# Kernel tuning notes

Measured on AMD Instinct MI355X. Metric: run time of the kernel, lower is better.

Reference implementation:

```python
import jax, jax.numpy as jnp
import numpy as np

N_TRAIN = 2000
N_ATOMS = 21
DIM_D = N_ATOMS * (N_ATOMS - 1) // 2   # 210 pairwise descriptors
DIM_I = 3 * N_ATOMS                    # 63 Cartesian force dims
N_PERMS = 12
N_COLS = 8
SIG = 10.0

_TRIL_ROWS, _TRIL_COLS = np.tril_indices(N_ATOMS, k=-1)


def setup_inputs() -> dict:
    key = jax.random.key(0)
    k1, k2 = jax.random.split(key)
    R_desc = jax.random.normal(k1, (N_TRAIN, DIM_D), dtype=jnp.float32)
    R_d_desc = jax.random.normal(k2, (N_TRAIN, DIM_D, 3), dtype=jnp.float32)
    rng = np.random.default_rng(0)
    # permutation table: identity first, then random symmetry perms of descriptor rows
    perms = np.stack([np.arange(DIM_D)] + [rng.permutation(DIM_D) for _ in range(N_PERMS - 1)])  # (P, D)
    # linear indices into a tiled (P copies) descriptor, laid out so that
    # tril_perms_lin.reshape(DIM_D, N_PERMS)[k, p] = perms[p, k] + p*DIM_D (matches sGDML)
    tril_perms_lin = (perms.T + np.arange(N_PERMS)[None, :] * DIM_D).ravel()
    j_idxs = rng.integers(0, N_TRAIN, size=N_COLS)
    return {
        "R_desc": R_desc,
        "R_d_desc": R_d_desc,
        "tril_perms_lin": jnp.asarray(tril_perms_lin, dtype=jnp.int32),
        "j_idxs": jnp.asarray(j_idxs, dtype=jnp.int32),
    }


def _d_desc_full(d_comp):
    """Expand compact pairwise Jacobian (N, D, 3) to full (N, D, 3*A).
    Pair row k for atoms (a,b) gets +d in atom a's slot and -d in atom b's slot."""
    n = d_comp.shape[0]
    out = jnp.zeros((n, DIM_D, N_ATOMS, 3), d_comp.dtype)
    k = jnp.arange(DIM_D)
    out = out.at[:, k, _TRIL_ROWS].set(d_comp)
    out = out.at[:, k, _TRIL_COLS].set(-d_comp)
    return out.reshape(n, DIM_D, DIM_I)


def reference(R_desc, R_d_desc, tril_perms_lin, j_idxs):
    sqrt5 = np.sqrt(5.0).astype(np.float32)
    base_div = 3.0 * SIG ** 4
    # indexing a P-fold tiled array of length D is equivalent to mod D
    perm_idx = jnp.reshape(tril_perms_lin, (DIM_D, N_PERMS)).T % DIM_D  # (P, D)
    Rd_full = _d_desc_full(R_d_desc)  # (N, D, I)

    def column_block(j):
        rj_desc_perms = R_desc[j][perm_idx]        # (P, D)  permuted descriptor of point j
        rj_d_perms = Rd_full[j][perm_idx]          # (P, D, I) permuted Jacobian of point j
        diff = R_desc[:, None, :] - rj_desc_perms[None, :, :]   # (N, P, D)
        norm = sqrt5 * jnp.linalg.norm(diff, axis=-1)            # (N, P)
        mat52 = jnp.exp(-norm / SIG) * (5.0 / base_div)          # (N, P)
        b = jnp.einsum('npd,pde->npe', diff, rj_d_perms)         # (N, P, I)
        outer = jnp.einsum('npd,npe->nde', diff * (5.0 * mat52)[..., None], b)  # (N, D, I)
        outer = outer - jnp.einsum('pde,np->nde', rj_d_perms, (SIG ** 2 + SIG * norm) * mat52)
        kblk = jnp.einsum('nde,ndk->nke', outer, Rd_full)        # (N, I_row, I_col)
        return kblk.reshape(N_TRAIN * DIM_I, DIM_I)

    K = jax.vmap(column_block)(j_idxs)                 # (nJ, N*I, I)
    K = jnp.transpose(K, (1, 0, 2)).reshape(N_TRAIN * DIM_I, N_COLS * DIM_I)
    return K
```

## Files before the change

kernel.cpp:

```cpp
#include <hip/hip_runtime.h>
#include <hip/hip_fp16.h>
#include <math.h>

#define NTRAIN 2000
#define DIMD 210
#define DIMI 63
#define NPERM 12
#define NCOLS 8
#define NATOM 21
#define SIGF 10.0f

#define WS_PERM      0
#define WS_PAIRROW   5040
#define WS_PAIRCOL   5250
#define WS_GTAB      6300
#define WS_ENTOFF    11340
#define WS_ENTS      11782
#define WS_TILEMAP   21862
#define WS_PERMAB    22304
#define A_INT_OFF    25088
#define A_BYTE_OFF   (A_INT_OFF * 4)
#define A_PER_N      (64 * 224)
#define A_BYTES      ((size_t)NTRAIN * A_PER_N * 2)
#define WS_NEEDED    ((size_t)A_BYTE_OFF + A_BYTES)

typedef _Float16 f16x8 __attribute__((ext_vector_type(8)));
typedef float f32x4 __attribute__((ext_vector_type(4)));

__global__ __launch_bounds__(512) void gdml_setup(const int* __restrict__ tril,
                                                  int* __restrict__ ws, int wsBig) {
  __shared__ int sPerm[NPERM * DIMD];
  __shared__ int sInv[NPERM * DIMD];
  __shared__ int sRow[DIMD], sCol[DIMD];
  __shared__ int sPairs[NATOM * 20], sNeg[NATOM * 20];
  __shared__ int sCnt[441];
  __shared__ int sScan[512];
  __shared__ int sOff[442];

  const int tid = threadIdx.x;

  for (int d = tid; d < DIMD; d += 512) {
    int a = 1;
    while ((a * (a + 1)) / 2 <= d) a++;
    sRow[d] = a;
    sCol[d] = d - (a * (a - 1)) / 2;
  }
  for (int idx = tid; idx < NPERM * DIMD; idx += 512) {
    int p = idx / DIMD, d = idx % DIMD;
    sPerm[idx] = tril[d * NPERM + p] % DIMD;
  }
  __syncthreads();
  for (int idx = tid; idx < NPERM * DIMD; idx += 512) {
    int p = idx / DIMD;
    sInv[p * DIMD + sPerm[idx]] = idx % DIMD;
  }
  if (tid < NATOM) {
    int t = tid, c = 0;
    for (int d = 0; d < DIMD; ++d) {
      if (sRow[d] == t)      { sPairs[t * 20 + c] = d; sNeg[t * 20 + c] = 0; c++; }
      else if (sCol[d] == t) { sPairs[t * 20 + c] = d; sNeg[t * 20 + c] = 1; c++; }
    }
  }
  __syncthreads();

  for (int idx = tid; idx < NPERM * DIMD; idx += 512) ws[WS_PERM + idx] = sPerm[idx];
  for (int d = tid; d < DIMD; d += 512) {
    ws[WS_PAIRROW + d] = sRow[d];
    ws[WS_PAIRCOL + d] = sCol[d];
  }
  for (int idx = tid; idx < NPERM * NATOM * 20; idx += 512) {
    int p = idx / (NATOM * 20);
    int r = idx % (NATOM * 20);
    int d = sPairs[r], neg = sNeg[r];
    int tw = sInv[p * DIMD + d];
    int pd = sPerm[p * DIMD + d];
    ws[WS_GTAB + idx] = d | (tw << 9) | (pd << 18) | (neg << 27);
  }
  if (wsBig) {
    for (int idx = tid; idx < NPERM * DIMD; idx += 512) {
      int dd = sPerm[idx];
      ws[WS_PERMAB + idx] = dd | (sRow[dd] << 8) | (sCol[dd] << 13);
    }
  }

  for (int q = tid; q < 441; q += 512) {
    int A = q / NATOM, B = q % NATOM, c = 0;
    for (int i = 0; i < 20; ++i) {
      int d = sPairs[A * 20 + i];
      for (int p = 0; p < NPERM; ++p) {
        int dd = sPerm[p * DIMD + d];
        c += (sRow[dd] == B) + (sCol[dd] == B);
      }
    }
    sCnt[q] = c;
  }
  __syncthreads();

  sScan[tid] = (tid < 441) ? sCnt[tid] : 0;
  __syncthreads();
  for (int s = 1; s < 512; s <<= 1) {
    int v = (tid >= s) ? sScan[tid - s] : 0;
    __syncthreads();
    sScan[tid] += v;
    __syncthreads();
  }
  if (tid == 0) sOff[0] = 0;
  if (tid < 441) sOff[tid + 1] = sScan[tid];
  __syncthreads();
  for (int q = tid; q < 442; q += 512) ws[WS_ENTOFF + q] = sOff[q];

  for (int q = tid; q < 441; q += 512) {
    int c = sCnt[q], r = 0;
    for (int q2 = 0; q2 < 441; ++q2) {
      int c2v = sCnt[q2];
      r += (c2v > c) || (c2v == c && q2 < q);
    }
    ws[WS_TILEMAP + r] = q;
  }

  for (int q = tid; q < 441; q += 512) {
    int A = q / NATOM, B = q % NATOM;
    int o = sOff[q];
    for (int i = 0; i < 20; ++i) {
      int d = sPairs[A * 20 + i];
      int negA = sNeg[A * 20 + i];
      for (int p = 0; p < NPERM; ++p) {
        int dd = sPerm[p * DIMD + d];
        int base = (d << 3) | (dd << 15) | (p << 26);
        if (sRow[dd] == B) ws[WS_ENTS + (o++)] = base | ((negA ^ 1) << 30);
        if (sCol[dd] == B) ws[WS_ENTS + (o++)] = base | (negA << 30);
      }
    }
  }
}

__global__ __launch_bounds__(256) void build_A(const float* __restrict__ R_d_desc,
                                               int* __restrict__ ws) {
  const int bid = blockIdx.x;
  const int n = (bid & 7) * (NTRAIN / 8) + (bid >> 3);
  const int* gtab = ws + WS_GTAB;
  _Float16* A = (_Float16*)((char*)ws + A_BYTE_OFF) + (size_t)n * A_PER_N;
  const float* rd = R_d_desc + (size_t)n * (DIMD * 3);
  const int tid = threadIdx.x;

  f16x8 z = {0, 0, 0, 0, 0, 0, 0, 0};
  for (int u = tid; u < 64 * 28; u += 256) ((f16x8*)A)[u] = z;
  __syncthreads();

  for (int u = tid; u < NATOM * 20; u += 256) {
    int v = gtab[u];
    int d = v & 511;
    float s = (v & (1 << 27)) ? -1.0f : 1.0f;
    int at = u / 20;
    A[(3 * at + 0) * 224 + d] = (_Float16)(s * rd[3 * d + 0]);
    A[(3 * at + 1) * 224 + d] = (_Float16)(s * rd[3 * d + 1]);
    A[(3 * at + 2) * 224 + d] = (_Float16)(s * rd[3 * d + 2]);
  }
}

__device__ inline unsigned h16(float f) {
  return (unsigned)__half_as_ushort(__float2half_rn(f));
}
__device__ inline float uh(unsigned u) {
  return __half2float(__ushort_as_half((unsigned short)(u & 0xFFFFu)));
}
__device__ inline int tswz(int r, int e) {
  return r * 64 + ((((e >> 3) ^ r) & 7) << 3) + (e & 7);
}
__device__ inline float pick3(uint2 v, int u) {
  return (u == 0) ? uh(v.x) : (u == 1) ? uh(v.x >> 16) : uh(v.y);
}

#define MT_STRIDE 232

__global__ __launch_bounds__(256, 4) void gdml_main_mfma(
    const float* __restrict__ R_desc, const float* __restrict__ R_d_desc,
    const int* __restrict__ j_idxs, const int* __restrict__ ws,
    float* __restrict__ out) {
  const int* perm   = ws + WS_PERM;
  const int* gtab   = ws + WS_GTAB;
  const int* permAB = ws + WS_PERMAB;

  const int bid = blockIdx.x;
  const int x = bid & 7;
  const int t = bid >> 3;
  const int n = x * (NTRAIN / 8) + (t >> 3);
  const int jc = t & 7;
  const int tid = threadIdx.x;
  const int j = j_idxs[jc];

  __shared__ __align__(16) _Float16 MT[64 * MT_STRIDE];
  __shared__ uint2 Rdn2[DIMD];
  __shared__ uint2 Rdj2[DIMD];
  __shared__ __align__(16) _Float16 Gk[64][16];
  __shared__ float c1s[NPERM], c2s[NPERM];
  __shared__ float Rn[DIMD], Rj[DIMD];
  __shared__ float partial[252];

  for (int i = tid; i < DIMD; i += 256) {
    Rn[i] = R_desc[(size_t)n * DIMD + i];
    Rj[i] = R_desc[(size_t)j * DIMD + i];
  }
  if (tid < DIMD) {
    const float* gn = R_d_desc + (size_t)n * (DIMD * 3) + 3 * tid;
    const float* gj = R_d_desc + (size_t)j * (DIMD * 3) + 3 * tid;
    Rdn2[tid] = make_uint2(h16(gn[0]) | (h16(gn[1]) << 16), h16(gn[2]));
    Rdj2[tid] = make_uint2(h16(gj[0]) | (h16(gj[1]) << 16), h16(gj[2]));
  }
  {
    float4 zf = make_float4(0.f, 0.f, 0.f, 0.f);
    float4* mz = (float4*)MT;
    for (int i = tid; i < 64 * MT_STRIDE * 2 / 16; i += 256) mz[i] = zf;
    f16x8 z8 = {0, 0, 0, 0, 0, 0, 0, 0};
    for (int i = tid; i < 128; i += 256) ((f16x8*)Gk)[i] = z8;
  }
  __syncthreads();

  if (tid < 252) {
    int p = tid / 21, seg = tid % 21;
    const int* pp = &perm[p * DIMD + seg * 10];
    const float* rn = &Rn[seg * 10];
    float s = 0.f;
#pragma unroll
    for (int i = 0; i < 10; ++i) {
      float v = rn[i] - Rj[pp[i]];
      s += v * v;
    }
    partial[tid] = s;
  }
  __syncthreads();
  if (tid < NPERM) {
    float s = 0.f;
#pragma unroll
    for (int i = 0; i < 21; ++i) s += partial[tid * 21 + i];
    float nrm = sqrtf(5.0f) * sqrtf(s);
    float mat52 = expf(-nrm / SIGF) * (5.0f / (3.0f * SIGF * SIGF * SIGF * SIGF));
    c1s[tid] = 5.0f * mat52;
    c2s[tid] = (SIGF * SIGF + SIGF * nrm) * mat52;
  }
  __syncthreads();

  if (tid < NPERM * NATOM) {
    int p = tid / NATOM, at = tid % NATOM;
    const int* gt = &gtab[(p * NATOM + at) * 20];
    float g0 = 0, g1 = 0, g2 = 0, b0 = 0, b1 = 0, b2 = 0;
#pragma unroll
    for (int i = 0; i < 20; ++i) {
      int v = gt[i];
      int d = v & 511, tw = (v >> 9) & 511, pd = (v >> 18) & 511;
      unsigned sg = ((unsigned)(v & (1 << 27))) << 4;
      float fd = __uint_as_float(__float_as_uint(Rn[d] - Rj[pd]) ^ sg);
      float ftw = __uint_as_float(__float_as_uint(Rn[tw] - Rj[d]) ^ sg);
      uint2 rn = Rdn2[d];
      uint2 rj = Rdj2[d];
      g0 += uh(rn.x) * fd;  g1 += uh(rn.x >> 16) * fd;  g2 += uh(rn.y) * fd;
      b0 += uh(rj.x) * ftw; b1 += uh(rj.x >> 16) * ftw; b2 += uh(rj.y) * ftw;
    }
    float c1 = c1s[p];
    Gk[3 * at + 0][4 + p] = (_Float16)(c1 * g0);
    Gk[3 * at + 1][4 + p] = (_Float16)(c1 * g1);
    Gk[3 * at + 2][4 + p] = (_Float16)(c1 * g2);
    MT[(3 * at + 0) * MT_STRIDE + 212 + p] = (_Float16)b0;
    MT[(3 * at + 1) * MT_STRIDE + 212 + p] = (_Float16)b1;
    MT[(3 * at + 2) * MT_STRIDE + 212 + p] = (_Float16)b2;
  }

  if (tid < DIMD) {
    int d = tid;
    _Float16* m = MT + d;
#pragma unroll
    for (int p = 0; p < NPERM; ++p) {
      int v = permAB[p * DIMD + d];
      int dd = v & 255, a = (v >> 8) & 31, b = (v >> 13) & 31;
      float c2 = c2s[p];
      uint2 rj = Rdj2[dd];
      float v0 = c2 * uh(rj.x), v1 = c2 * uh(rj.x >> 16), v2 = c2 * uh(rj.y);
      int ca = (3 * a) * MT_STRIDE, cb = (3 * b) * MT_STRIDE;
      m[ca] = (_Float16)((float)m[ca] - v0);
      m[ca + MT_STRIDE] = (_Float16)((float)m[ca + MT_STRIDE] - v1);
      m[ca + 2 * MT_STRIDE] = (_Float16)((float)m[ca + 2 * MT_STRIDE] - v2);
      m[cb] = (_Float16)((float)m[cb] + v0);
      m[cb + MT_STRIDE] = (_Float16)((float)m[cb + MT_STRIDE] + v1);
      m[cb + 2 * MT_STRIDE] = (_Float16)((float)m[cb + 2 * MT_STRIDE] + v2);
    }
  } else {
    for (int r = tid - DIMD; r < DIMI; r += 256 - DIMD) {
      int at = r / 3, u = r - 3 * at;
      float v208 = (at == 20) ? pick3(Rdn2[208], u)
                 : (at == 18) ? -pick3(Rdn2[208], u) : 0.f;
      float v209 = (at == 20) ? pick3(Rdn2[209], u)
                 : (at == 19) ? -pick3(Rdn2[209], u) : 0.f;
      Gk[r][0] = (_Float16)v208;
      Gk[r][1] = (_Float16)v209;
    }
  }
  __syncthreads();

  f32x4 acc0 = {0.f, 0.f, 0.f, 0.f}, acc1 = acc0, acc2 = acc0, acc3 = acc0;
  const int lane = tid & 63;
  const int nt = tid >> 6;
  const int ci = lane & 15;
  const int kOct = lane >> 4;
  {
    const _Float16* Ag = (const _Float16*)((const char*)ws + A_BYTE_OFF)
                         + (size_t)n * A_PER_N;
    const _Float16* aBase = Ag + ci * 224 + kOct * 8;
    const _Float16* mBase = &MT[(16 * nt + ci) * MT_STRIDE + kOct * 8];
#pragma unroll
    for (int kk = 0; kk < 7; ++kk) {
      f16x8 bf = *(const f16x8*)(mBase + kk * 32);
      f16x8 a0, a1, a2, a3;
      if (kk == 6 && kOct >= 2) {
        int off = (kOct - 2) * 8;
        a0 = *(const f16x8*)&Gk[ci][off];
        a1 = *(const f16x8*)&Gk[16 + ci][off];
        a2 = *(const f16x8*)&Gk[32 + ci][off];
        a3 = *(const f16x8*)&Gk[48 + ci][off];
      } else {
        a0 = *(const f16x8*)(aBase + kk * 32);
        a1 = *(const f16x8*)(aBase + 16 * 224 + kk * 32);
        a2 = *(const f16x8*)(aBase + 32 * 224 + kk * 32);
        a3 = *(const f16x8*)(aBase + 48 * 224 + kk * 32);
      }
      acc0 = __builtin_amdgcn_mfma_f32_16x16x32_f16(a0, bf, acc0, 0, 0, 0);
      acc1 = __builtin_amdgcn_mfma_f32_16x16x32_f16(a1, bf, acc1, 0, 0, 0);
      acc2 = __builtin_amdgcn_mfma_f32_16x16x32_f16(a2, bf, acc2, 0, 0, 0);
      acc3 = __builtin_amdgcn_mfma_f32_16x16x32_f16(a3, bf, acc3, 0, 0, 0);
    }
  }

  {
    const int c = 16 * nt + ci;
    if (c < DIMI) {
      const size_t base = (size_t)n * DIMI * (NCOLS * DIMI) + (size_t)jc * DIMI;
      float* ob = out + base + c;
      const int rb = kOct * 4;
#pragma unroll
      for (int r8 = 0; r8 < 4; ++r8) {
        int r = rb + r8;
        ob[(size_t)r * (NCOLS * DIMI)] = acc0[r8];
        ob[(size_t)(16 + r) * (NCOLS * DIMI)] = acc1[r8];
        ob[(size_t)(32 + r) * (NCOLS * DIMI)] = acc2[r8];
        if (48 + r < DIMI) ob[(size_t)(48 + r) * (NCOLS * DIMI)] = acc3[r8];
      }
    }
  }
}

__global__ __launch_bounds__(256, 8) void gdml_main_csr(
    const float* __restrict__ R_desc, const float* __restrict__ R_d_desc,
    const int* __restrict__ j_idxs, const int* __restrict__ ws,
    float* __restrict__ out) {
  const int* perm    = ws + WS_PERM;
  const int* gtab    = ws + WS_GTAB;
  const int* entOff  = ws + WS_ENTOFF;
  const int* ents    = ws + WS_ENTS;
  const int* tileMap = ws + WS_TILEMAP;

  const int bid = blockIdx.x;
  const int jc = bid & 7;
  const int n = bid >> 3;
  const int tid = threadIdx.x;
  const int j = j_idxs[jc];

  __shared__ uint2 Rdn2[DIMD];
  __shared__ uint2 Rdj2[DIMD];
  __shared__ __align__(16) float GT[NPERM][64];
  __shared__ __align__(16) float bT[NPERM][64];
  __shared__ float c1s[NPERM], c2s[NPERM];
  __shared__ __align__(16) char uni[DIMI * 64 * 2];
  float* Rn = (float*)uni;
  float* Rj = Rn + DIMD;
  float* partial = Rj + DIMD;
  ushort* tileH = (ushort*)uni;

  for (int i = tid; i < DIMD; i += 256) {
    Rn[i] = R_desc[(size_t)n * DIMD + i];
    Rj[i] = R_desc[(size_t)j * DIMD + i];
  }
  if (tid < DIMD) {
    const float* gn = R_d_desc + (size_t)n * (DIMD * 3) + 3 * tid;
    const float* gj = R_d_desc + (size_t)j * (DIMD * 3) + 3 * tid;
    Rdn2[tid] = make_uint2(h16(gn[0]) | (h16(gn[1]) << 16), h16(gn[2]));
    Rdj2[tid] = make_uint2(h16(gj[0]) | (h16(gj[1]) << 16), h16(gj[2]));
  }
  __syncthreads();

  if (tid < 252) {
    int p = tid / 21, seg = tid % 21;
    const int* pp = &perm[p * DIMD + seg * 10];
    const float* rn = &Rn[seg * 10];
    float s = 0.f;
#pragma unroll
    for (int i = 0; i < 10; ++i) {
      float v = rn[i] - Rj[pp[i]];
      s += v * v;
    }
    partial[tid] = s;
  }
  __syncthreads();
  if (tid < NPERM) {
    float s = 0.f;
#pragma unroll
    for (int i = 0; i < 21; ++i) s += partial[tid * 21 + i];
    float nrm = sqrtf(5.0f) * sqrtf(s);
    float mat52 = expf(-nrm / SIGF) * (5.0f / (3.0f * SIGF * SIGF * SIGF * SIGF));
    c1s[tid] = 5.0f * mat52;
    c2s[tid] = (SIGF * SIGF + SIGF * nrm) * mat52;
  }
  __syncthreads();

  if (tid < NPERM * NATOM) {
    int p = tid / NATOM, at = tid % NATOM;
    const int* gt = &gtab[(p * NATOM + at) * 20];
    float g0 = 0, g1 = 0, g2 = 0, b0 = 0, b1 = 0, b2 = 0;
#pragma unroll
    for (int i = 0; i < 20; ++i) {
      int v = gt[i];
      int d = v & 511, tw = (v >> 9) & 511, pd = (v >> 18) & 511;
      unsigned sg = ((unsigned)(v & (1 << 27))) << 4;
      float fd = __uint_as_float(__float_as_uint(Rn[d] - Rj[pd]) ^ sg);
      float ftw = __uint_as_float(__float_as_uint(Rn[tw] - Rj[d]) ^ sg);
      uint2 rn = Rdn2[d];
      uint2 rj = Rdj2[d];
      g0 += uh(rn.x) * fd;  g1 += uh(rn.x >> 16) * fd;  g2 += uh(rn.y) * fd;
      b0 += uh(rj.x) * ftw; b1 += uh(rj.x >> 16) * ftw; b2 += uh(rj.y) * ftw;
    }
    float c1 = c1s[p];
    GT[p][3 * at + 0] = c1 * g0;
    GT[p][3 * at + 1] = c1 * g1;
    GT[p][3 * at + 2] = c1 * g2;
    bT[p][3 * at + 0] = b0;
    bT[p][3 * at + 1] = b1;
    bT[p][3 * at + 2] = b2;
  }
  __syncthreads();

  for (int s = 0; s < 2; ++s) {
    int rank;
    if (s == 0) { if (tid > 220) break; rank = tid; }
    else        { if (tid >= 220) break; rank = 440 - tid; }
    int q = tileMap[rank];
    int A = q / NATOM, B = q % NATOM;
    float acc[3][3];
#pragma unroll
    for (int c = 0; c < 3; ++c)
#pragma unroll
      for (int e = 0; e < 3; ++e) acc[c][e] = 0.f;

    int o0 = entOff[q], o1 = entOff[q + 1];
    for (int o = o0; o < o1; ++o) {
      int v = ents[o];
      int d8  = v & 0xFF8;
      int dd8 = (v >> 12) & 0xFF8;
      int p4  = (v >> 24) & 0x3C;
      unsigned sgn = ((unsigned)v & 0x40000000u) << 1;
      float c2 = __uint_as_float(
          __float_as_uint(*(const float*)((const char*)c2s + p4)) ^ sgn);
      uint2 rn = *(const uint2*)((const char*)Rdn2 + d8);
      uint2 rj = *(const uint2*)((const char*)Rdj2 + dd8);
      float nx = uh(rn.x), ny = uh(rn.x >> 16), nz = uh(rn.y);
      float w0 = c2 * uh(rj.x), w1 = c2 * uh(rj.x >> 16), w2 = c2 * uh(rj.y);
      acc[0][0] += nx * w0; acc[0][1] += nx * w1; acc[0][2] += nx * w2;
      acc[1][0] += ny * w0; acc[1][1] += ny * w1; acc[1][2] += ny * w2;
      acc[2][0] += nz * w0; acc[2][1] += nz * w1; acc[2][2] += nz * w2;
    }
#pragma unroll
    for (int cg = 0; cg < 3; ++cg) {
      int r = 3 * A + cg;
#pragma unroll
      for (int u = 0; u < 3; ++u)
        tileH[tswz(r, 3 * B + u)] = (ushort)h16(acc[cg][u]);
    }
  }
  __syncthreads();

  const size_t base = (size_t)n * DIMI * (NCOLS * DIMI) + (size_t)jc * DIMI;
  if (tid < 252) {
    int k = tid >> 2, ec = tid & 3;
    int e0 = ec * 16;
    const uint4* q0 = (const uint4*)&tileH[k * 64 + (((2 * ec) ^ k) & 7) * 8];
    const uint4* q1 = (const uint4*)&tileH[k * 64 + (((2 * ec + 1) ^ k) & 7) * 8];
    uint4 u0 = *q0, u1 = *q1;
    float acc[16];
    acc[0] = uh(u0.x);  acc[1] = uh(u0.x >> 16);
    acc[2] = uh(u0.y);  acc[3] = uh(u0.y >> 16);
    acc[4] = uh(u0.z);  acc[5] = uh(u0.z >> 16);
    acc[6] = uh(u0.w);  acc[7] = uh(u0.w >> 16);
    acc[8] = uh(u1.x);  acc[9] = uh(u1.x >> 16);
    acc[10] = uh(u1.y); acc[11] = uh(u1.y >> 16);
    acc[12] = uh(u1.z); acc[13] = uh(u1.z >> 16);
    acc[14] = uh(u1.w); acc[15] = uh(u1.w >> 16);
#pragma unroll
    for (int p = 0; p < NPERM; ++p) {
      float g = GT[p][k];
      const float4* bp = (const float4*)&bT[p][e0];
      float4 b0 = bp[0], b1 = bp[1], b2 = bp[2], b3 = bp[3];
      acc[0] += g * b0.x;  acc[1] += g * b0.y;  acc[2] += g * b0.z;  acc[3] += g * b0.w;
      acc[4] += g * b1.x;  acc[5] += g * b1.y;  acc[6] += g * b1.z;  acc[7] += g * b1.w;
      acc[8] += g * b2.x;  acc[9] += g * b2.y;  acc[10] += g * b2.z; acc[11] += g * b2.w;
      acc[12] += g * b3.x; acc[13] += g * b3.y; acc[14] += g * b3.z; acc[15] += g * b3.w;
    }
    float* op = out + base + (size_t)k * (NCOLS * DIMI) + e0;
    const int lim = DIMI - e0;
#pragma unroll
    for (int i = 0; i < 16; ++i)
      if (i < lim) op[i] = acc[i];
  }
}

extern "C" void kernel_launch(void* const* d_in, const int* in_sizes, int n_in,
                              void* d_out, int out_size, void* d_ws, size_t ws_size,
                              hipStream_t stream) {
  const float* R_desc = (const float*)d_in[0];
  const float* R_d_desc = (const float*)d_in[1];
  const int* tril = (const int*)d_in[2];
  const int* j_idxs = (const int*)d_in[3];
  float* out = (float*)d_out;
  int* ws = (int*)d_ws;

  const int wsBig = (ws_size >= WS_NEEDED) ? 1 : 0;
  hipLaunchKernelGGL(gdml_setup, dim3(1), dim3(512), 0, stream, tril, ws, wsBig);
  if (wsBig) {
    hipLaunchKernelGGL(build_A, dim3(NTRAIN), dim3(256), 0, stream, R_d_desc, ws);
    hipLaunchKernelGGL(gdml_main_mfma, dim3(NTRAIN * NCOLS), dim3(256), 0, stream,
                       R_desc, R_d_desc, j_idxs, ws, out);
  } else {
    hipLaunchKernelGGL(gdml_main_csr, dim3(NTRAIN * NCOLS), dim3(256), 0, stream,
                       R_desc, R_d_desc, j_idxs, ws, out);
  }
}
```

Before: 341.7 us.

## Fuse permuted-norm reduction into gtab pass and software-pipeline MFMA loads

```diff
diff --git a/kernel.cpp b/kernel.cpp
--- a/kernel.cpp
+++ b/kernel.cpp
@@ -177,7 +177,6 @@
     const float* __restrict__ R_desc, const float* __restrict__ R_d_desc,
     const int* __restrict__ j_idxs, const int* __restrict__ ws,
     float* __restrict__ out) {
-  const int* perm   = ws + WS_PERM;
   const int* gtab   = ws + WS_GTAB;
   const int* permAB = ws + WS_PERMAB;
 
@@ -194,14 +193,12 @@
   __shared__ uint2 Rdj2[DIMD];
   __shared__ __align__(16) _Float16 Gk[64][16];
   __shared__ float c1s[NPERM], c2s[NPERM];
-  __shared__ float Rn[DIMD], Rj[DIMD];
+  __shared__ float2 RnRj[DIMD];
   __shared__ float partial[252];
 
-  for (int i = tid; i < DIMD; i += 256) {
-    Rn[i] = R_desc[(size_t)n * DIMD + i];
-    Rj[i] = R_desc[(size_t)j * DIMD + i];
-  }
   if (tid < DIMD) {
+    RnRj[tid] = make_float2(R_desc[(size_t)n * DIMD + tid],
+                            R_desc[(size_t)j * DIMD + tid]);
     const float* gn = R_d_desc + (size_t)n * (DIMD * 3) + 3 * tid;
     const float* gj = R_d_desc + (size_t)j * (DIMD * 3) + 3 * tid;
     Rdn2[tid] = make_uint2(h16(gn[0]) | (h16(gn[1]) << 16), h16(gn[2]));
@@ -216,23 +213,37 @@
   }
   __syncthreads();
 
-  if (tid < 252) {
-    int p = tid / 21, seg = tid % 21;
-    const int* pp = &perm[p * DIMD + seg * 10];
-    const float* rn = &Rn[seg * 10];
-    float s = 0.f;
-#pragma unroll
-    for (int i = 0; i < 10; ++i) {
-      float v = rn[i] - Rj[pp[i]];
-      s += v * v;
-    }
-    partial[tid] = s;
-  }
-  __syncthreads();
+  float g0 = 0, g1 = 0, g2 = 0, b0 = 0, b1 = 0, b2 = 0;
+  int bp = 0, bat = 0;
+  if (tid < NPERM * NATOM) {
+    bp = tid / NATOM; bat = tid - bp * NATOM;
+    const int* gt = &gtab[(bp * NATOM + bat) * 20];
+    float nacc = 0.f;
+#pragma unroll
+    for (int i = 0; i < 20; ++i) {
+      int v = gt[i];
+      int d = v & 511, tw = (v >> 9) & 511, pd = (v >> 18) & 511;
+      unsigned sg = ((unsigned)(v & (1 << 27))) << 4;
+      float2 rrd = RnRj[d];
+      float diff_d = rrd.x - RnRj[pd].y;
+      float diff_tw = RnRj[tw].x - rrd.y;
+      float fd = __uint_as_float(__float_as_uint(diff_d) ^ sg);
+      float ftw = __uint_as_float(__float_as_uint(diff_tw) ^ sg);
+      nacc += diff_d * diff_d;
+      uint2 rn = Rdn2[d];
+      uint2 rj = Rdj2[d];
+      g0 += uh(rn.x) * fd;  g1 += uh(rn.x >> 16) * fd;  g2 += uh(rn.y) * fd;
+      b0 += uh(rj.x) * ftw; b1 += uh(rj.x >> 16) * ftw; b2 += uh(rj.y) * ftw;
+    }
+    partial[tid] = nacc;
+  }
+  __syncthreads();
+
   if (tid < NPERM) {
     float s = 0.f;
 #pragma unroll
     for (int i = 0; i < 21; ++i) s += partial[tid * 21 + i];
+    s *= 0.5f;
     float nrm = sqrtf(5.0f) * sqrtf(s);
     float mat52 = expf(-nrm / SIGF) * (5.0f / (3.0f * SIGF * SIGF * SIGF * SIGF));
     c1s[tid] = 5.0f * mat52;
@@ -241,30 +252,14 @@
   __syncthreads();
 
   if (tid < NPERM * NATOM) {
-    int p = tid / NATOM, at = tid % NATOM;
-    const int* gt = &gtab[(p * NATOM + at) * 20];
-    float g0 = 0, g1 = 0, g2 = 0, b0 = 0, b1 = 0, b2 = 0;
-#pragma unroll
-    for (int i = 0; i < 20; ++i) {
-      int v = gt[i];
-      int d = v & 511, tw = (v >> 9) & 511, pd = (v >> 18) & 511;
-      unsigned sg = ((unsigned)(v & (1 << 27))) << 4;
-      float fd = __uint_as_float(__float_as_uint(Rn[d] - Rj[pd]) ^ sg);
-      float ftw = __uint_as_float(__float_as_uint(Rn[tw] - Rj[d]) ^ sg);
-      uint2 rn = Rdn2[d];
-      uint2 rj = Rdj2[d];
-      g0 += uh(rn.x) * fd;  g1 += uh(rn.x >> 16) * fd;  g2 += uh(rn.y) * fd;
-      b0 += uh(rj.x) * ftw; b1 += uh(rj.x >> 16) * ftw; b2 += uh(rj.y) * ftw;
-    }
-    float c1 = c1s[p];
-    Gk[3 * at + 0][4 + p] = (_Float16)(c1 * g0);
-    Gk[3 * at + 1][4 + p] = (_Float16)(c1 * g1);
-    Gk[3 * at + 2][4 + p] = (_Float16)(c1 * g2);
-    MT[(3 * at + 0) * MT_STRIDE + 212 + p] = (_Float16)b0;
-    MT[(3 * at + 1) * MT_STRIDE + 212 + p] = (_Float16)b1;
-    MT[(3 * at + 2) * MT_STRIDE + 212 + p] = (_Float16)b2;
-  }
-
+    float c1 = c1s[bp];
+    Gk[3 * bat + 0][4 + bp] = (_Float16)(c1 * g0);
+    Gk[3 * bat + 1][4 + bp] = (_Float16)(c1 * g1);
+    Gk[3 * bat + 2][4 + bp] = (_Float16)(c1 * g2);
+    MT[(3 * bat + 0) * MT_STRIDE + 212 + bp] = (_Float16)b0;
+    MT[(3 * bat + 1) * MT_STRIDE + 212 + bp] = (_Float16)b1;
+    MT[(3 * bat + 2) * MT_STRIDE + 212 + bp] = (_Float16)b2;
+  }
   if (tid < DIMD) {
     int d = tid;
     _Float16* m = MT + d;
@@ -301,32 +296,52 @@
   const int nt = tid >> 6;
   const int ci = lane & 15;
   const int kOct = lane >> 4;
+  const _Float16* Ag = (const _Float16*)((const char*)ws + A_BYTE_OFF)
+                       + (size_t)n * A_PER_N;
+  const _Float16* aBase = Ag + ci * 224 + kOct * 8;
+  const _Float16* mBase = &MT[(16 * nt + ci) * MT_STRIDE + kOct * 8];
   {
-    const _Float16* Ag = (const _Float16*)((const char*)ws + A_BYTE_OFF)
-                         + (size_t)n * A_PER_N;
-    const _Float16* aBase = Ag + ci * 224 + kOct * 8;
-    const _Float16* mBase = &MT[(16 * nt + ci) * MT_STRIDE + kOct * 8];
-#pragma unroll
-    for (int kk = 0; kk < 7; ++kk) {
-      f16x8 bf = *(const f16x8*)(mBase + kk * 32);
-      f16x8 a0, a1, a2, a3;
-      if (kk == 6 && kOct >= 2) {
-        int off = (kOct - 2) * 8;
-        a0 = *(const f16x8*)&Gk[ci][off];
-        a1 = *(const f16x8*)&Gk[16 + ci][off];
-        a2 = *(const f16x8*)&Gk[32 + ci][off];
-        a3 = *(const f16x8*)&Gk[48 + ci][off];
-      } else {
-        a0 = *(const f16x8*)(aBase + kk * 32);
-        a1 = *(const f16x8*)(aBase + 16 * 224 + kk * 32);
-        a2 = *(const f16x8*)(aBase + 32 * 224 + kk * 32);
-        a3 = *(const f16x8*)(aBase + 48 * 224 + kk * 32);
+    f16x8 bf_c = *(const f16x8*)(mBase);
+    f16x8 a0_c = *(const f16x8*)(aBase);
+    f16x8 a1_c = *(const f16x8*)(aBase + 16 * 224);
+    f16x8 a2_c = *(const f16x8*)(aBase + 32 * 224);
+    f16x8 a3_c = *(const f16x8*)(aBase + 48 * 224);
+#pragma unroll
+    for (int kk = 0; kk < 6; ++kk) {
+      f16x8 bf_n, a0_n, a1_n, a2_n, a3_n;
+      if (kk < 5) {
+        bf_n = *(const f16x8*)(mBase + (kk + 1) * 32);
+        a0_n = *(const f16x8*)(aBase + (kk + 1) * 32);
+        a1_n = *(const f16x8*)(aBase + 16 * 224 + (kk + 1) * 32);
+        a2_n = *(const f16x8*)(aBase + 32 * 224 + (kk + 1) * 32);
+        a3_n = *(const f16x8*)(aBase + 48 * 224 + (kk + 1) * 32);
       }
-      acc0 = __builtin_amdgcn_mfma_f32_16x16x32_f16(a0, bf, acc0, 0, 0, 0);
-      acc1 = __builtin_amdgcn_mfma_f32_16x16x32_f16(a1, bf, acc1, 0, 0, 0);
-      acc2 = __builtin_amdgcn_mfma_f32_16x16x32_f16(a2, bf, acc2, 0, 0, 0);
-      acc3 = __builtin_amdgcn_mfma_f32_16x16x32_f16(a3, bf, acc3, 0, 0, 0);
-    }
+      acc0 = __builtin_amdgcn_mfma_f32_16x16x32_f16(a0_c, bf_c, acc0, 0, 0, 0);
+      acc1 = __builtin_amdgcn_mfma_f32_16x16x32_f16(a1_c, bf_c, acc1, 0, 0, 0);
+      acc2 = __builtin_amdgcn_mfma_f32_16x16x32_f16(a2_c, bf_c, acc2, 0, 0, 0);
+      acc3 = __builtin_amdgcn_mfma_f32_16x16x32_f16(a3_c, bf_c, acc3, 0, 0, 0);
+      if (kk < 5) {
+        bf_c = bf_n; a0_c = a0_n; a1_c = a1_n; a2_c = a2_n; a3_c = a3_n;
+      }
+    }
+    f16x8 bf6 = *(const f16x8*)(mBase + 6 * 32);
+    f16x8 a0, a1, a2, a3;
+    if (kOct >= 2) {
+      int off = (kOct - 2) * 8;
+      a0 = *(const f16x8*)&Gk[ci][off];
+      a1 = *(const f16x8*)&Gk[16 + ci][off];
+      a2 = *(const f16x8*)&Gk[32 + ci][off];
+      a3 = *(const f16x8*)&Gk[48 + ci][off];
+    } else {
+      a0 = *(const f16x8*)(aBase + 6 * 32);
+      a1 = *(const f16x8*)(aBase + 16 * 224 + 6 * 32);
+      a2 = *(const f16x8*)(aBase + 32 * 224 + 6 * 32);
+      a3 = *(const f16x8*)(aBase + 48 * 224 + 6 * 32);
+    }
+    acc0 = __builtin_amdgcn_mfma_f32_16x16x32_f16(a0, bf6, acc0, 0, 0, 0);
+    acc1 = __builtin_amdgcn_mfma_f32_16x16x32_f16(a1, bf6, acc1, 0, 0, 0);
+    acc2 = __builtin_amdgcn_mfma_f32_16x16x32_f16(a2, bf6, acc2, 0, 0, 0);
+    acc3 = __builtin_amdgcn_mfma_f32_16x16x32_f16(a3, bf6, acc3, 0, 0, 0);
   }
 
   {
```

Measured after the change: 339.8 us. Within noise of the previous version (-0.6%).
